# Kernel optimization log

Measured on AMD Instinct MI355X. Metric: run time of the kernel, lower is better.

## Reference

```python
import jax, jax.numpy as jnp
import numpy as np

H = 128   # hidden_size
B = 8
TQ = 512  # num queries
TK = 512  # num keys


def setup_inputs() -> dict:
    key = jax.random.key(0)
    ks = jax.random.split(key, 8)
    s = 1.0 / np.sqrt(H)  # torch Linear default init bound
    return {
        "queries": jax.random.normal(ks[0], (B, TQ, H), dtype=jnp.float32),
        "keys": jax.random.normal(ks[1], (B, TK, H), dtype=jnp.float32),
        "Wa_w": jax.random.uniform(ks[2], (H, H), jnp.float32, -s, s),
        "Wa_b": jax.random.uniform(ks[3], (H,), jnp.float32, -s, s),
        "Ua_w": jax.random.uniform(ks[4], (H, H), jnp.float32, -s, s),
        "Ua_b": jax.random.uniform(ks[5], (H,), jnp.float32, -s, s),
        "Va_w": jax.random.uniform(ks[6], (H,), jnp.float32, -s, s),
        "Va_b": jax.random.uniform(ks[7], (), jnp.float32, -s, s),
    }


def reference(queries, keys, Wa_w, Wa_b, Ua_w, Ua_b, Va_w, Va_b):
    # Linear projections (torch Linear: y = x @ W.T + b)
    q = queries @ Wa_w.T + Wa_b                  # (B, Tq, H)
    k = keys @ Ua_w.T + Ua_b                     # (B, Tk, H)
    # Additive (Bahdanau) scores with broadcast intermediate (B, Tq, Tk, H)
    e = jnp.tanh(q[:, :, None, :] + k[:, None, :, :])
    scores = jnp.einsum('bqkh,h->bqk', e, Va_w) + Va_b  # (B, Tq, Tk)
    weights = jax.nn.softmax(scores, axis=-1)            # softmax over keys
    contexts = jnp.einsum('bqk,bkh->bqh', weights, keys) # (B, Tq, H)
    return contexts, weights
```

## Files before the change

### kernel.cpp

```cpp
#include <hip/hip_runtime.h>
#include <hip/hip_bf16.h>
#include <stdint.h>

#define HD 128
#define NB 8
#define TQN 512
#define TKN 512
#define QT 8
#define KTILE 64
#define KSTR 132
#define QSTR 132
#define KBSTR 136

typedef __attribute__((ext_vector_type(8))) short short8;
typedef __attribute__((ext_vector_type(4))) float f32x4;

static __device__ __forceinline__ float lo16(uint32_t w){
  union { uint32_t i; float f; } v; v.i = w << 16; return v.f;
}
static __device__ __forceinline__ float hi16(uint32_t w){
  union { uint32_t i; float f; } v; v.i = w & 0xffff0000u; return v.f;
}
static __device__ __forceinline__ float bf2f(unsigned short u){
  union { uint32_t i; float f; } v; v.i = ((uint32_t)u) << 16; return v.f;
}
static __device__ __forceinline__ uint32_t f2bf(float f){
  union { float f; uint32_t i; } v; v.f = f;
  uint32_t u = v.i;
  u += 0x7fffu + ((u >> 16) & 1u);
  return u >> 16;
}
static __device__ __forceinline__ float tanh_acc(float x){
  float e = __builtin_amdgcn_exp2f(x * 2.8853900817779268f);
  return fmaf(-2.0f, __builtin_amdgcn_rcpf(e + 1.0f), 1.0f);
}
template<int CTRL>
static __device__ __forceinline__ float dpp_add(float x){
  union { float f; int i; } u; u.f = x;
  int y = __builtin_amdgcn_update_dpp(0, u.i, CTRL, 0xf, 0xf, true);
  union { int i; float f; } w; w.i = y;
  return x + w.f;
}
static __device__ __forceinline__ float ld1(const void* p, size_t idx, bool f32){
  return f32 ? ((const float*)p)[idx] : bf2f(((const unsigned short*)p)[idx]);
}
static __device__ __forceinline__ short8 ld8bf(const void* p, size_t idx, bool f32){
  short8 r;
  if (f32){
    const float* s = (const float*)p + idx;
    #pragma unroll
    for (int i = 0; i < 8; i++) r[i] = (short)f2bf(s[i]);
  } else {
    r = *(const short8*)((const unsigned short*)p + idx);
  }
  return r;
}

__global__ __launch_bounds__(256) void proj_kernel(
    const void* __restrict__ queries, const void* __restrict__ keys,
    const void* __restrict__ Wa_w,   const void* __restrict__ Wa_b,
    const void* __restrict__ Ua_w,   const void* __restrict__ Ua_b,
    float* __restrict__ tq_g, float* __restrict__ tk_g)
{
  __shared__ unsigned int flg_s[8];
  const int tid = threadIdx.x;
  if (tid < 8) flg_s[tid] = 0;
  __syncthreads();
  {
    const void* ptrs[6] = {queries, keys, Wa_w, Wa_b, Ua_w, Ua_b};
    const int grp = tid >> 5;
    const int l   = tid & 31;
    if (grp < 6){
      const unsigned short* p = (const unsigned short*)ptrs[grp];
      unsigned short a = p[2*l], c = p[64 + 2*l];
      if (((a >> 7) & 0xFF) > 0x90 || ((c >> 7) & 0xFF) > 0x90)
        atomicOr(&flg_s[grp], 1u);
    }
  }
  __syncthreads();
  const int lane = tid & 63, wv = tid >> 6, ln = lane & 15, quad = lane >> 4;
  const int row0 = blockIdx.x * 16;

  const void* x; const void* W; const void* bias; float* dst; int r;
  bool fx, fw, fb;
  if (row0 < NB*TQN){
    x = queries; W = Wa_w; bias = Wa_b; dst = tq_g; r = row0;
    fx = flg_s[0] != 0; fw = flg_s[2] != 0; fb = flg_s[3] != 0;
  } else {
    x = keys; W = Ua_w; bias = Ua_b; dst = tk_g; r = row0 - NB*TQN;
    fx = flg_s[1] != 0; fw = flg_s[4] != 0; fb = flg_s[5] != 0;
  }

  short8 a[4];
  #pragma unroll
  for (int ks = 0; ks < 4; ks++)
    a[ks] = ld8bf(x, (size_t)(r + ln)*HD + ks*32 + quad*8, fx);

  #pragma unroll
  for (int nt = 0; nt < 2; nt++){
    const int h0 = (2*wv + nt)*16;
    f32x4 c = {0.f,0.f,0.f,0.f};
    #pragma unroll
    for (int ks = 0; ks < 4; ks++)
      c = __builtin_amdgcn_mfma_f32_16x16x32_bf16(
            a[ks], ld8bf(W, (size_t)(h0 + ln)*HD + ks*32 + quad*8, fw), c, 0,0,0);
    const float wb = ld1(bias, h0 + ln, fb);
    #pragma unroll
    for (int r4 = 0; r4 < 4; r4++)
      dst[(size_t)(r + quad*4 + r4)*HD + h0 + ln] = tanh_acc(c[r4] + wb);
  }
}

__global__ __launch_bounds__(512, 6) void attn_kernel(
    const void* __restrict__ queries, const void* __restrict__ keys,
    const void* __restrict__ Va_w,
    const float* __restrict__ tq_g, const float* __restrict__ tk_g,
    void* __restrict__ out)
{
  __shared__ __align__(16) float tk_s[KTILE*KSTR];
  __shared__ float sc_s[QT*TKN];
  __shared__ unsigned int flg_s[4];

  const int tid = threadIdx.x;
  if (tid < 4) flg_s[tid] = 0;
  __syncthreads();
  {
    const void* ptrs[3] = {queries, keys, Va_w};
    const int grp = tid >> 5;
    const int l   = tid & 31;
    if (grp < 3){
      const unsigned short* p = (const unsigned short*)ptrs[grp];
      unsigned short a = p[2*l], c = p[64 + 2*l];
      if (((a >> 7) & 0xFF) > 0x90 || ((c >> 7) & 0xFF) > 0x90)
        atomicOr(&flg_s[grp], 1u);
    }
  }
  __syncthreads();
  const bool fQ  = flg_s[0] != 0;
  const bool fK  = flg_s[1] != 0;
  const bool fVw = flg_s[2] != 0;

  const int lane = tid & 63;
  const int wv   = tid >> 6;
  const int ln   = lane & 15;
  const int quad = lane >> 4;
  const int s8   = lane >> 3;
  const int o8   = lane & 7;
  const int b     = blockIdx.x >> 6;
  const int qbase = (blockIdx.x & 63) * QT;

  float var[16], tqr[16];
  {
    #pragma unroll
    for (int j = 0; j < 16; j++) var[j] = ld1(Va_w, o8*16 + j, fVw);
    const float4* qsrc = (const float4*)(tq_g + (size_t)(b*TQN + qbase + wv)*HD + o8*16);
    #pragma unroll
    for (int c = 0; c < 4; c++){
      float4 t = qsrc[c];
      tqr[c*4+0]=t.x; tqr[c*4+1]=t.y; tqr[c*4+2]=t.z; tqr[c*4+3]=t.w;
    }
  }

  float sc8[8];
  for (int kt = 0; kt < 8; kt++){
    {
      const float4* src = (const float4*)(tk_g + (size_t)(b*TKN + kt*KTILE)*HD);
      #pragma unroll
      for (int j = 0; j < 4; j++){
        const int f = tid + 512*j;
        const int k = f >> 5;
        const int h = (f & 31) * 4;
        *(float4*)(tk_s + k*KSTR + h) = src[f];
      }
    }
    __syncthreads();

    float acc[8];
    #pragma unroll
    for (int i = 0; i < 8; i++) acc[i] = 0.f;
    #pragma unroll
    for (int i = 0; i < 8; i++){
      const float* tk = tk_s + (i*8 + s8)*KSTR + o8*16;
      #pragma unroll
      for (int c = 0; c < 4; c++){
        const float4 kv = *(const float4*)(tk + c*4);
        acc[i] = fmaf(var[c*4+0]*(tqr[c*4+0]+kv.x),
                      __builtin_amdgcn_rcpf(fmaf(tqr[c*4+0], kv.x, 1.f)), acc[i]);
        acc[i] = fmaf(var[c*4+1]*(tqr[c*4+1]+kv.y),
                      __builtin_amdgcn_rcpf(fmaf(tqr[c*4+1], kv.y, 1.f)), acc[i]);
        acc[i] = fmaf(var[c*4+2]*(tqr[c*4+2]+kv.z),
                      __builtin_amdgcn_rcpf(fmaf(tqr[c*4+2], kv.z, 1.f)), acc[i]);
        acc[i] = fmaf(var[c*4+3]*(tqr[c*4+3]+kv.w),
                      __builtin_amdgcn_rcpf(fmaf(tqr[c*4+3], kv.w, 1.f)), acc[i]);
      }
    }
    #pragma unroll
    for (int i = 0; i < 8; i++){
      float a = acc[i];
      a = dpp_add<0xB1>(a);
      a = dpp_add<0x4E>(a);
      a = dpp_add<0x141>(a);
      acc[i] = a;
    }
    float sc = acc[0];
    #pragma unroll
    for (int i = 1; i < 8; i++) sc = (o8 == i) ? acc[i] : sc;
    sc8[kt] = sc;
    __syncthreads();
  }

  {
    float m = sc8[0];
    #pragma unroll
    for (int j = 1; j < 8; j++) m = fmaxf(m, sc8[j]);
    #pragma unroll
    for (int o = 32; o > 0; o >>= 1) m = fmaxf(m, __shfl_xor(m, o));
    float sum = 0.f;
    #pragma unroll
    for (int j = 0; j < 8; j++){
      sc8[j] = __builtin_amdgcn_exp2f((sc8[j]-m)*1.4426950408889634f);
      sum += sc8[j];
    }
    #pragma unroll
    for (int o = 32; o > 0; o >>= 1) sum += __shfl_xor(sum, o);
    const float inv = __builtin_amdgcn_rcpf(sum);
    const size_t wbase = (size_t)NB*TQN*HD + (size_t)(b*TQN + qbase + wv)*TKN;
    #pragma unroll
    for (int j = 0; j < 8; j++){
      const float w = sc8[j]*inv;
      const int kk = j*KTILE + o8*8 + s8;
      sc_s[wv*TKN + kk] = w;
      if (fQ) ((float*)out)[wbase + kk] = w;
      else    ((unsigned short*)out)[wbase + kk] = (unsigned short)f2bf(w);
    }
  }
  __syncthreads();

  {
    const int p2 = wv & 3;
    const int g2 = wv >> 2;
    const int h0 = ln * 8;
    float a0[8], a1[8];
    #pragma unroll
    for (int t = 0; t < 8; t++){ a0[t] = 0.f; a1[t] = 0.f; }
    for (int kt = 0; kt < 8; kt++){
      if (fK){
        const float4* src = (const float4*)((const float*)keys + (size_t)(b*TKN + kt*KTILE)*HD);
        #pragma unroll
        for (int j = 0; j < 4; j++){
          const int f = tid + 512*j;
          const int k = f >> 5;
          const int h = (f & 31) * 4;
          *(float4*)(tk_s + k*KSTR + h) = src[f];
        }
      } else {
        const uint4* src = (const uint4*)((const unsigned short*)keys + (size_t)(b*TKN + kt*KTILE)*HD);
        #pragma unroll
        for (int j = 0; j < 2; j++){
          const int f = tid + 512*j;
          const int k = f >> 4;
          const int h = (f & 15) * 8;
          uint4 v = src[f];
          float4 d0, d1;
          d0.x = lo16(v.x); d0.y = hi16(v.x); d0.z = lo16(v.y); d0.w = hi16(v.y);
          d1.x = lo16(v.z); d1.y = hi16(v.z); d1.z = lo16(v.w); d1.w = hi16(v.w);
          *(float4*)(tk_s + k*KSTR + h)     = d0;
          *(float4*)(tk_s + k*KSTR + h + 4) = d1;
        }
      }
      __syncthreads();
      const float* w0r = sc_s + (2*p2)*TKN + kt*KTILE + g2*32;
      const float* w1r = w0r + TKN;
      #pragma unroll
      for (int i = 0; i < 8; i++){
        const int k = i*4 + quad;
        const float w0 = w0r[k];
        const float w1 = w1r[k];
        const float* kr = tk_s + (g2*32 + k)*KSTR + h0;
        const float4 k0 = *(const float4*)(kr);
        const float4 k1 = *(const float4*)(kr + 4);
        a0[0]=fmaf(w0,k0.x,a0[0]); a0[1]=fmaf(w0,k0.y,a0[1]);
        a0[2]=fmaf(w0,k0.z,a0[2]); a0[3]=fmaf(w0,k0.w,a0[3]);
        a0[4]=fmaf(w0,k1.x,a0[4]); a0[5]=fmaf(w0,k1.y,a0[5]);
        a0[6]=fmaf(w0,k1.z,a0[6]); a0[7]=fmaf(w0,k1.w,a0[7]);
        a1[0]=fmaf(w1,k0.x,a1[0]); a1[1]=fmaf(w1,k0.y,a1[1]);
        a1[2]=fmaf(w1,k0.z,a1[2]); a1[3]=fmaf(w1,k0.w,a1[3]);
        a1[4]=fmaf(w1,k1.x,a1[4]); a1[5]=fmaf(w1,k1.y,a1[5]);
        a1[6]=fmaf(w1,k1.z,a1[6]); a1[7]=fmaf(w1,k1.w,a1[7]);
      }
      __syncthreads();
    }
    #pragma unroll
    for (int t = 0; t < 8; t++){
      a0[t] += __shfl_xor(a0[t], 16); a0[t] += __shfl_xor(a0[t], 32);
      a1[t] += __shfl_xor(a1[t], 16); a1[t] += __shfl_xor(a1[t], 32);
    }
    float* part = sc_s;
    if (g2 == 1 && quad == 0){
      *(float4*)(part + (2*p2  )*HD + h0    ) = (float4){a0[0],a0[1],a0[2],a0[3]};
      *(float4*)(part + (2*p2  )*HD + h0 + 4) = (float4){a0[4],a0[5],a0[6],a0[7]};
      *(float4*)(part + (2*p2+1)*HD + h0    ) = (float4){a1[0],a1[1],a1[2],a1[3]};
      *(float4*)(part + (2*p2+1)*HD + h0 + 4) = (float4){a1[4],a1[5],a1[6],a1[7]};
    }
    __syncthreads();
    if (g2 == 0 && quad == 0){
      const float4 p00 = *(const float4*)(part + (2*p2  )*HD + h0    );
      const float4 p01 = *(const float4*)(part + (2*p2  )*HD + h0 + 4);
      const float4 p10 = *(const float4*)(part + (2*p2+1)*HD + h0    );
      const float4 p11 = *(const float4*)(part + (2*p2+1)*HD + h0 + 4);
      const size_t crow0 = (size_t)(b*TQN + qbase + 2*p2    )*HD + h0;
      const size_t crow1 = (size_t)(b*TQN + qbase + 2*p2 + 1)*HD + h0;
      if (fQ){
        float* oc = (float*)out;
        *(float4*)(oc + crow0)     = (float4){a0[0]+p00.x, a0[1]+p00.y, a0[2]+p00.z, a0[3]+p00.w};
        *(float4*)(oc + crow0 + 4) = (float4){a0[4]+p01.x, a0[5]+p01.y, a0[6]+p01.z, a0[7]+p01.w};
        *(float4*)(oc + crow1)     = (float4){a1[0]+p10.x, a1[1]+p10.y, a1[2]+p10.z, a1[3]+p10.w};
        *(float4*)(oc + crow1 + 4) = (float4){a1[4]+p11.x, a1[5]+p11.y, a1[6]+p11.z, a1[7]+p11.w};
      } else {
        uint4 o0, o1;
        o0.x = f2bf(a0[0]+p00.x) | (f2bf(a0[1]+p00.y) << 16);
        o0.y = f2bf(a0[2]+p00.z) | (f2bf(a0[3]+p00.w) << 16);
        o0.z = f2bf(a0[4]+p01.x) | (f2bf(a0[5]+p01.y) << 16);
        o0.w = f2bf(a0[6]+p01.z) | (f2bf(a0[7]+p01.w) << 16);
        o1.x = f2bf(a1[0]+p10.x) | (f2bf(a1[1]+p10.y) << 16);
        o1.y = f2bf(a1[2]+p10.z) | (f2bf(a1[3]+p10.w) << 16);
        o1.z = f2bf(a1[4]+p11.x) | (f2bf(a1[5]+p11.y) << 16);
        o1.w = f2bf(a1[6]+p11.z) | (f2bf(a1[7]+p11.w) << 16);
        *(uint4*)((unsigned short*)out + crow0) = o0;
        *(uint4*)((unsigned short*)out + crow1) = o1;
      }
    }
  }
}

__global__ __launch_bounds__(512, 4) void fused_kernel(
    const void* __restrict__ queries, const void* __restrict__ keys,
    const void* __restrict__ Wa_w,   const void* __restrict__ Wa_b,
    const void* __restrict__ Ua_w,   const void* __restrict__ Ua_b,
    const void* __restrict__ Va_w,
    void* __restrict__ out)
{
  __shared__ float qp_s[QT*QSTR];
  __shared__ float va_s[HD];
  __shared__ __align__(16) unsigned short keys_s[KTILE*KBSTR];
  __shared__ __align__(16) float kp_s[KTILE*KSTR];
  __shared__ float sc_s[QT*TKN];
  __shared__ unsigned int flg_s[8];

  const int tid = threadIdx.x;
  if (tid < 8) flg_s[tid] = 0;
  __syncthreads();
  {
    const void* ptrs[7] = {queries, keys, Wa_w, Wa_b, Ua_w, Ua_b, Va_w};
    const int grp = tid >> 5;
    const int l   = tid & 31;
    if (grp < 7){
      const unsigned short* p = (const unsigned short*)ptrs[grp];
      unsigned short a = p[2*l], c = p[64 + 2*l];
      if (((a >> 7) & 0xFF) > 0x90 || ((c >> 7) & 0xFF) > 0x90)
        atomicOr(&flg_s[grp], 1u);
    }
  }
  __syncthreads();
  const bool fQ  = flg_s[0] != 0;
  const bool fK  = flg_s[1] != 0;
  const bool fWw = flg_s[2] != 0;
  const bool fWb = flg_s[3] != 0;
  const bool fUw = flg_s[4] != 0;
  const bool fUb = flg_s[5] != 0;
  const bool fVw = flg_s[6] != 0;

  const int lane = tid & 63;
  const int wv   = tid >> 6;
  const int ln   = lane & 15;
  const int quad = lane >> 4;
  const int b     = blockIdx.x >> 6;
  const int qbase = (blockIdx.x & 63) * QT;

  if (tid < HD) va_s[tid] = ld1(Va_w, tid, fVw);
  {
    const int h0 = wv * 16;
    const size_t qrow = (size_t)(b*TQN + qbase + (ln & 7))*HD;
    f32x4 c = {0.f,0.f,0.f,0.f};
    #pragma unroll
    for (int ks = 0; ks < 4; ks++){
      short8 a = ld8bf(queries, qrow + ks*32 + quad*8, fQ);
      short8 w = ld8bf(Wa_w, (size_t)(h0 + ln)*HD + ks*32 + quad*8, fWw);
      c = __builtin_amdgcn_mfma_f32_16x16x32_bf16(a, w, c, 0,0,0);
    }
    const float wb = ld1(Wa_b, h0 + ln, fWb);
    #pragma unroll
    for (int r = 0; r < 4; r++){
      const int row = quad*4 + r;
      if (row < QT) qp_s[row*QSTR + h0 + ln] = tanh_acc(c[r] + wb);
    }
  }
  short8 ub[4];
  float ubias;
  {
    const int h0 = wv * 16;
    #pragma unroll
    for (int ks = 0; ks < 4; ks++)
      ub[ks] = ld8bf(Ua_w, (size_t)(h0 + ln)*HD + ks*32 + quad*8, fUw);
    ubias = ld1(Ua_b, h0 + ln, fUb);
  }
  {
    if (fK){
      const float4* src = (const float4*)((const float*)keys + (size_t)(b*TKN)*HD);
      #pragma unroll
      for (int j = 0; j < 4; j++){
        const int f = tid + 512*j;
        float4 v = src[f];
        const int k = f >> 5, h = (f & 31)*4;
        uint2 p;
        p.x = f2bf(v.x) | (f2bf(v.y) << 16);
        p.y = f2bf(v.z) | (f2bf(v.w) << 16);
        *(uint2*)(keys_s + k*KBSTR + h) = p;
      }
    } else {
      const uint4* src = (const uint4*)((const unsigned short*)keys + (size_t)(b*TKN)*HD);
      #pragma unroll
      for (int j = 0; j < 2; j++){
        const int f = tid + 512*j;
        uint4 v = src[f];
        const int k = f >> 4, h = (f & 15)*8;
        *(uint4*)(keys_s + k*KBSTR + h) = v;
      }
    }
  }
  __syncthreads();

  const int s8 = lane >> 3;
  const int o8 = lane & 7;
  float tqr[16], var[16], vat[16];
  {
    const float* qsrc = qp_s + wv*QSTR + o8*16;
    const float* vsrc = va_s + o8*16;
    #pragma unroll
    for (int c = 0; c < 4; c++){
      float4 t = *(const float4*)(qsrc + c*4);
      float4 v = *(const float4*)(vsrc + c*4);
      tqr[c*4+0]=t.x; tqr[c*4+1]=t.y; tqr[c*4+2]=t.z; tqr[c*4+3]=t.w;
      var[c*4+0]=v.x; var[c*4+1]=v.y; var[c*4+2]=v.z; var[c*4+3]=v.w;
      vat[c*4+0]=v.x*t.x; vat[c*4+1]=v.y*t.y; vat[c*4+2]=v.z*t.z; vat[c*4+3]=v.w*t.w;
    }
  }
  for (int kt = 0; kt < 8; kt++){
    f32x4 kc[4];
    #pragma unroll
    for (int mt = 0; mt < 4; mt++) kc[mt] = (f32x4){0.f,0.f,0.f,0.f};
    #pragma unroll
    for (int ks = 0; ks < 4; ks++){
      short8 af[4];
      #pragma unroll
      for (int mt = 0; mt < 4; mt++)
        af[mt] = *(const short8*)(keys_s + (mt*16 + ln)*KBSTR + ks*32 + quad*8);
      #pragma unroll
      for (int mt = 0; mt < 4; mt++)
        kc[mt] = __builtin_amdgcn_mfma_f32_16x16x32_bf16(af[mt], ub[ks], kc[mt], 0,0,0);
    }
    __syncthreads();
    #pragma unroll
    for (int mt = 0; mt < 4; mt++)
      #pragma unroll
      for (int r = 0; r < 4; r++)
        kp_s[(mt*16 + quad*4 + r)*KSTR + wv*16 + ln] = tanh_acc(kc[mt][r] + ubias);
    if (kt < 7){
      if (fK){
        const float4* src = (const float4*)((const float*)keys + (size_t)(b*TKN + (kt+1)*KTILE)*HD);
        #pragma unroll
        for (int j = 0; j < 4; j++){
          const int f = tid + 512*j;
          float4 v = src[f];
          const int k = f >> 5, h = (f & 31)*4;
          uint2 p;
          p.x = f2bf(v.x) | (f2bf(v.y) << 16);
          p.y = f2bf(v.z) | (f2bf(v.w) << 16);
          *(uint2*)(keys_s + k*KBSTR + h) = p;
        }
      } else {
        const uint4* src = (const uint4*)((const unsigned short*)keys + (size_t)(b*TKN + (kt+1)*KTILE)*HD);
        #pragma unroll
        for (int j = 0; j < 2; j++){
          const int f = tid + 512*j;
          uint4 v = src[f];
          const int k = f >> 4, h = (f & 15)*8;
          *(uint4*)(keys_s + k*KBSTR + h) = v;
        }
      }
    }
    __syncthreads();
    float acc[8];
    #pragma unroll
    for (int i = 0; i < 8; i++) acc[i] = 0.f;
    #pragma unroll
    for (int i = 0; i < 8; i++){
      const float* tk = kp_s + (i*8 + s8)*KSTR + o8*16;
      #pragma unroll
      for (int c = 0; c < 4; c++){
        const float4 kv = *(const float4*)(tk + c*4);
        acc[i] = fmaf(fmaf(var[c*4+0], kv.x, vat[c*4+0]),
                      __builtin_amdgcn_rcpf(fmaf(tqr[c*4+0], kv.x, 1.f)), acc[i]);
        acc[i] = fmaf(fmaf(var[c*4+1], kv.y, vat[c*4+1]),
                      __builtin_amdgcn_rcpf(fmaf(tqr[c*4+1], kv.y, 1.f)), acc[i]);
        acc[i] = fmaf(fmaf(var[c*4+2], kv.z, vat[c*4+2]),
                      __builtin_amdgcn_rcpf(fmaf(tqr[c*4+2], kv.z, 1.f)), acc[i]);
        acc[i] = fmaf(fmaf(var[c*4+3], kv.w, vat[c*4+3]),
                      __builtin_amdgcn_rcpf(fmaf(tqr[c*4+3], kv.w, 1.f)), acc[i]);
      }
    }
    #pragma unroll
    for (int i = 0; i < 8; i++){
      float a = acc[i];
      a = dpp_add<0xB1>(a);
      a = dpp_add<0x4E>(a);
      a = dpp_add<0x141>(a);
      acc[i] = a;
    }
    float sc = acc[0];
    #pragma unroll
    for (int i = 1; i < 8; i++) sc = (o8 == i) ? acc[i] : sc;
    sc_s[wv*TKN + kt*KTILE + o8*8 + s8] = sc;
  }
  __syncthreads();
  {
    float vals[8];
    float m = -1e30f;
    #pragma unroll
    for (int j = 0; j < 8; j++){
      vals[j] = sc_s[wv*TKN + lane + 64*j];
      m = fmaxf(m, vals[j]);
    }
    #pragma unroll
    for (int o = 32; o > 0; o >>= 1) m = fmaxf(m, __shfl_xor(m, o));
    float sum = 0.f;
    #pragma unroll
    for (int j = 0; j < 8; j++){
      vals[j] = __builtin_amdgcn_exp2f((vals[j]-m)*1.4426950408889634f);
      sum += vals[j];
    }
    #pragma unroll
    for (int o = 32; o > 0; o >>= 1) sum += __shfl_xor(sum, o);
    const float inv = __builtin_amdgcn_rcpf(sum);
    const size_t wbase = (size_t)NB*TQN*HD + (size_t)(b*TQN + qbase + wv)*TKN;
    #pragma unroll
    for (int j = 0; j < 8; j++){
      const float w = vals[j]*inv;
      sc_s[wv*TKN + lane + 64*j] = w;
      if (fQ) ((float*)out)[wbase + lane + 64*j] = w;
      else    ((unsigned short*)out)[wbase + lane + 64*j] = (unsigned short)f2bf(w);
    }
  }
  __syncthreads();
  {
    const int p2 = wv & 3;
    const int g2 = wv >> 2;
    const int h0 = ln * 8;
    float a0[8], a1[8];
    #pragma unroll
    for (int t = 0; t < 8; t++){ a0[t] = 0.f; a1[t] = 0.f; }
    for (int kt = 0; kt < 8; kt++){
      if (fK){
        const float4* src = (const float4*)((const float*)keys + (size_t)(b*TKN + kt*KTILE)*HD);
        #pragma unroll
        for (int j = 0; j < 4; j++){
          const int f = tid + 512*j;
          const int k = f >> 5, h = (f & 31)*4;
          *(float4*)(kp_s + k*KSTR + h) = src[f];
        }
      } else {
        const uint4* src = (const uint4*)((const unsigned short*)keys + (size_t)(b*TKN + kt*KTILE)*HD);
        #pragma unroll
        for (int j = 0; j < 2; j++){
          const int f = tid + 512*j;
          const int k = f >> 4, h = (f & 15)*8;
          uint4 v = src[f];
          float4 d0, d1;
          d0.x = lo16(v.x); d0.y = hi16(v.x); d0.z = lo16(v.y); d0.w = hi16(v.y);
          d1.x = lo16(v.z); d1.y = hi16(v.z); d1.z = lo16(v.w); d1.w = hi16(v.w);
          *(float4*)(kp_s + k*KSTR + h)     = d0;
          *(float4*)(kp_s + k*KSTR + h + 4) = d1;
        }
      }
      __syncthreads();
      const float* w0r = sc_s + (2*p2)*TKN + kt*KTILE + g2*32;
      const float* w1r = w0r + TKN;
      #pragma unroll
      for (int i = 0; i < 8; i++){
        const int k = i*4 + quad;
        const float w0 = w0r[k];
        const float w1 = w1r[k];
        const float* kr = kp_s + (g2*32 + k)*KSTR + h0;
        const float4 k0 = *(const float4*)(kr);
        const float4 k1 = *(const float4*)(kr + 4);
        a0[0]=fmaf(w0,k0.x,a0[0]); a0[1]=fmaf(w0,k0.y,a0[1]);
        a0[2]=fmaf(w0,k0.z,a0[2]); a0[3]=fmaf(w0,k0.w,a0[3]);
        a0[4]=fmaf(w0,k1.x,a0[4]); a0[5]=fmaf(w0,k1.y,a0[5]);
        a0[6]=fmaf(w0,k1.z,a0[6]); a0[7]=fmaf(w0,k1.w,a0[7]);
        a1[0]=fmaf(w1,k0.x,a1[0]); a1[1]=fmaf(w1,k0.y,a1[1]);
        a1[2]=fmaf(w1,k0.z,a1[2]); a1[3]=fmaf(w1,k0.w,a1[3]);
        a1[4]=fmaf(w1,k1.x,a1[4]); a1[5]=fmaf(w1,k1.y,a1[5]);
        a1[6]=fmaf(w1,k1.z,a1[6]); a1[7]=fmaf(w1,k1.w,a1[7]);
      }
      __syncthreads();
    }
    #pragma unroll
    for (int t = 0; t < 8; t++){
      a0[t] += __shfl_xor(a0[t], 16); a0[t] += __shfl_xor(a0[t], 32);
      a1[t] += __shfl_xor(a1[t], 16); a1[t] += __shfl_xor(a1[t], 32);
    }
    float* part = qp_s;
    if (g2 == 1 && quad == 0){
      *(float4*)(part + (2*p2  )*HD + h0    ) = (float4){a0[0],a0[1],a0[2],a0[3]};
      *(float4*)(part + (2*p2  )*HD + h0 + 4) = (float4){a0[4],a0[5],a0[6],a0[7]};
      *(float4*)(part + (2*p2+1)*HD + h0    ) = (float4){a1[0],a1[1],a1[2],a1[3]};
      *(float4*)(part + (2*p2+1)*HD + h0 + 4) = (float4){a1[4],a1[5],a1[6],a1[7]};
    }
    __syncthreads();
    if (g2 == 0 && quad == 0){
      const float4 p00 = *(const float4*)(part + (2*p2  )*HD + h0    );
      const float4 p01 = *(const float4*)(part + (2*p2  )*HD + h0 + 4);
      const float4 p10 = *(const float4*)(part + (2*p2+1)*HD + h0    );
      const float4 p11 = *(const float4*)(part + (2*p2+1)*HD + h0 + 4);
      const size_t crow0 = (size_t)(b*TQN + qbase + 2*p2    )*HD + h0;
      const size_t crow1 = (size_t)(b*TQN + qbase + 2*p2 + 1)*HD + h0;
      if (fQ){
        float* oc = (float*)out;
        *(float4*)(oc + crow0)     = (float4){a0[0]+p00.x, a0[1]+p00.y, a0[2]+p00.z, a0[3]+p00.w};
        *(float4*)(oc + crow0 + 4) = (float4){a0[4]+p01.x, a0[5]+p01.y, a0[6]+p01.z, a0[7]+p01.w};
        *(float4*)(oc + crow1)     = (float4){a1[0]+p10.x, a1[1]+p10.y, a1[2]+p10.z, a1[3]+p10.w};
        *(float4*)(oc + crow1 + 4) = (float4){a1[4]+p11.x, a1[5]+p11.y, a1[6]+p11.z, a1[7]+p11.w};
      } else {
        uint4 o0, o1;
        o0.x = f2bf(a0[0]+p00.x) | (f2bf(a0[1]+p00.y) << 16);
        o0.y = f2bf(a0[2]+p00.z) | (f2bf(a0[3]+p00.w) << 16);
        o0.z = f2bf(a0[4]+p01.x) | (f2bf(a0[5]+p01.y) << 16);
        o0.w = f2bf(a0[6]+p01.z) | (f2bf(a0[7]+p01.w) << 16);
        o1.x = f2bf(a1[0]+p10.x) | (f2bf(a1[1]+p10.y) << 16);
        o1.y = f2bf(a1[2]+p10.z) | (f2bf(a1[3]+p10.w) << 16);
        o1.z = f2bf(a1[4]+p11.x) | (f2bf(a1[5]+p11.y) << 16);
        o1.w = f2bf(a1[6]+p11.z) | (f2bf(a1[7]+p11.w) << 16);
        *(uint4*)((unsigned short*)out + crow0) = o0;
        *(uint4*)((unsigned short*)out + crow1) = o1;
      }
    }
  }
}

extern "C" void kernel_launch(void* const* d_in, const int* in_sizes, int n_in,
                              void* d_out, int out_size, void* d_ws, size_t ws_size,
                              hipStream_t stream) {
  (void)in_sizes; (void)n_in; (void)out_size;
  const size_t need = (size_t)2 * NB * TQN * HD * sizeof(float);
  if (ws_size >= need){
    float* tq_g = (float*)d_ws;
    float* tk_g = tq_g + (size_t)NB*TQN*HD;
    proj_kernel<<<512, 256, 0, stream>>>(d_in[0], d_in[1], d_in[2], d_in[3],
                                         d_in[4], d_in[5], tq_g, tk_g);
    attn_kernel<<<512, 512, 0, stream>>>(d_in[0], d_in[1], d_in[6],
                                         tq_g, tk_g, d_out);
  } else {
    fused_kernel<<<512, 512, 0, stream>>>(d_in[0], d_in[1], d_in[2], d_in[3],
                                          d_in[4], d_in[5], d_in[6], d_out);
  }
}
```

Measured before the change: 156.0 us.

## Prefetch key tiles into registers, use packed FMA math, interleave batches across blocks

Tiles of projected keys and raw keys are now prefetched into registers while the current tile is being computed, so global loads overlap with compute. The score and context inner loops use two-wide float vectors, which lets the compiler emit packed FMA, and the score numerator is algebraically refactored to var*k + var*q. Block indexing is interleaved by batch, softmax weights are transposed with ds_bpermute to give coalesced stores, and the occupancy hint drops from 6 to 4 blocks to leave registers for the prefetch buffers. The risks are higher register pressure and lower occupancy.

```diff
diff --git a/kernel.cpp b/kernel.cpp
--- a/kernel.cpp
+++ b/kernel.cpp
@@ -14,6 +14,13 @@
 
 typedef __attribute__((ext_vector_type(8))) short short8;
 typedef __attribute__((ext_vector_type(4))) float f32x4;
+typedef __attribute__((ext_vector_type(2))) float f32x2;
+
+#if __has_builtin(__builtin_elementwise_fma)
+#define FMA2(a,b,c) __builtin_elementwise_fma((a),(b),(c))
+#else
+#define FMA2(a,b,c) ((a)*(b)+(c))
+#endif
 
 static __device__ __forceinline__ float lo16(uint32_t w){
   union { uint32_t i; float f; } v; v.i = w << 16; return v.f;
@@ -79,7 +86,10 @@
   }
   __syncthreads();
   const int lane = tid & 63, wv = tid >> 6, ln = lane & 15, quad = lane >> 4;
-  const int row0 = blockIdx.x * 16;
+  const int b7  = blockIdx.x & 7;
+  const int idx = blockIdx.x >> 3;
+  const int row0 = (idx < 32) ? (b7*TQN + idx*16)
+                              : (NB*TQN + b7*TKN + (idx-32)*16);
 
   const void* x; const void* W; const void* bias; float* dst; int r;
   bool fx, fw, fb;
@@ -111,7 +121,7 @@
   }
 }
 
-__global__ __launch_bounds__(512, 6) void attn_kernel(
+__global__ __launch_bounds__(512, 4) void attn_kernel(
     const void* __restrict__ queries, const void* __restrict__ keys,
     const void* __restrict__ Va_w,
     const float* __restrict__ tq_g, const float* __restrict__ tk_g,
@@ -122,6 +132,16 @@
   __shared__ unsigned int flg_s[4];
 
   const int tid = threadIdx.x;
+  const int b     = blockIdx.x & 7;
+  const int qbase = (blockIdx.x >> 3) * QT;
+
+  float4 st[4];
+  {
+    const float4* src = (const float4*)(tk_g + (size_t)(b*TKN)*HD);
+    #pragma unroll
+    for (int j = 0; j < 4; j++) st[j] = src[tid + 512*j];
+  }
+
   if (tid < 4) flg_s[tid] = 0;
   __syncthreads();
   {
@@ -146,67 +166,87 @@
   const int quad = lane >> 4;
   const int s8   = lane >> 3;
   const int o8   = lane & 7;
-  const int b     = blockIdx.x >> 6;
-  const int qbase = (blockIdx.x & 63) * QT;
-
-  float var[16], tqr[16];
-  {
-    #pragma unroll
-    for (int j = 0; j < 16; j++) var[j] = ld1(Va_w, o8*16 + j, fVw);
+
+  f32x2 var2[8], tq2[8], vat2[8];
+  {
+    float vtmp[16];
+    #pragma unroll
+    for (int j = 0; j < 16; j++) vtmp[j] = ld1(Va_w, o8*16 + j, fVw);
     const float4* qsrc = (const float4*)(tq_g + (size_t)(b*TQN + qbase + wv)*HD + o8*16);
     #pragma unroll
     for (int c = 0; c < 4; c++){
       float4 t = qsrc[c];
-      tqr[c*4+0]=t.x; tqr[c*4+1]=t.y; tqr[c*4+2]=t.z; tqr[c*4+3]=t.w;
-    }
-  }
+      f32x2 t0; t0.x = t.x; t0.y = t.y;
+      f32x2 t1; t1.x = t.z; t1.y = t.w;
+      f32x2 v0; v0.x = vtmp[4*c+0]; v0.y = vtmp[4*c+1];
+      f32x2 v1; v1.x = vtmp[4*c+2]; v1.y = vtmp[4*c+3];
+      tq2[2*c] = t0;  tq2[2*c+1] = t1;
+      var2[2*c] = v0; var2[2*c+1] = v1;
+      vat2[2*c] = v0 * t0; vat2[2*c+1] = v1 * t1;
+    }
+  }
+  f32x2 one2; one2.x = 1.f; one2.y = 1.f;
 
   float sc8[8];
   for (int kt = 0; kt < 8; kt++){
-    {
-      const float4* src = (const float4*)(tk_g + (size_t)(b*TKN + kt*KTILE)*HD);
-      #pragma unroll
-      for (int j = 0; j < 4; j++){
-        const int f = tid + 512*j;
-        const int k = f >> 5;
-        const int h = (f & 31) * 4;
-        *(float4*)(tk_s + k*KSTR + h) = src[f];
-      }
+    #pragma unroll
+    for (int j = 0; j < 4; j++){
+      const int f = tid + 512*j;
+      *(float4*)(tk_s + (f >> 5)*KSTR + (f & 31)*4) = st[j];
     }
     __syncthreads();
-
-    float acc[8];
-    #pragma unroll
-    for (int i = 0; i < 8; i++) acc[i] = 0.f;
+    if (kt < 7){
+      const float4* src = (const float4*)(tk_g + (size_t)(b*TKN + (kt+1)*KTILE)*HD);
+      #pragma unroll
+      for (int j = 0; j < 4; j++) st[j] = src[tid + 512*j];
+    }
+
+    f32x2 acc2[8];
+    #pragma unroll
+    for (int i = 0; i < 8; i++){ acc2[i].x = 0.f; acc2[i].y = 0.f; }
     #pragma unroll
     for (int i = 0; i < 8; i++){
       const float* tk = tk_s + (i*8 + s8)*KSTR + o8*16;
       #pragma unroll
       for (int c = 0; c < 4; c++){
         const float4 kv = *(const float4*)(tk + c*4);
-        acc[i] = fmaf(var[c*4+0]*(tqr[c*4+0]+kv.x),
-                      __builtin_amdgcn_rcpf(fmaf(tqr[c*4+0], kv.x, 1.f)), acc[i]);
-        acc[i] = fmaf(var[c*4+1]*(tqr[c*4+1]+kv.y),
-                      __builtin_amdgcn_rcpf(fmaf(tqr[c*4+1], kv.y, 1.f)), acc[i]);
-        acc[i] = fmaf(var[c*4+2]*(tqr[c*4+2]+kv.z),
-                      __builtin_amdgcn_rcpf(fmaf(tqr[c*4+2], kv.z, 1.f)), acc[i]);
-        acc[i] = fmaf(var[c*4+3]*(tqr[c*4+3]+kv.w),
-                      __builtin_amdgcn_rcpf(fmaf(tqr[c*4+3], kv.w, 1.f)), acc[i]);
-      }
-    }
+        f32x2 kv0; kv0.x = kv.x; kv0.y = kv.y;
+        f32x2 kv1; kv1.x = kv.z; kv1.y = kv.w;
+        f32x2 n0 = FMA2(var2[2*c],   kv0, vat2[2*c]);
+        f32x2 d0 = FMA2(tq2[2*c],    kv0, one2);
+        f32x2 n1 = FMA2(var2[2*c+1], kv1, vat2[2*c+1]);
+        f32x2 d1 = FMA2(tq2[2*c+1],  kv1, one2);
+        f32x2 r0; r0.x = __builtin_amdgcn_rcpf(d0.x); r0.y = __builtin_amdgcn_rcpf(d0.y);
+        f32x2 r1; r1.x = __builtin_amdgcn_rcpf(d1.x); r1.y = __builtin_amdgcn_rcpf(d1.y);
+        acc2[i] = FMA2(n0, r0, acc2[i]);
+        acc2[i] = FMA2(n1, r1, acc2[i]);
+      }
+    }
+    float ar[8];
     #pragma unroll
     for (int i = 0; i < 8; i++){
-      float a = acc[i];
+      float a = acc2[i].x + acc2[i].y;
       a = dpp_add<0xB1>(a);
       a = dpp_add<0x4E>(a);
       a = dpp_add<0x141>(a);
-      acc[i] = a;
-    }
-    float sc = acc[0];
-    #pragma unroll
-    for (int i = 1; i < 8; i++) sc = (o8 == i) ? acc[i] : sc;
+      ar[i] = a;
+    }
+    float sc = ar[0];
+    #pragma unroll
+    for (int i = 1; i < 8; i++) sc = (o8 == i) ? ar[i] : sc;
     sc8[kt] = sc;
     __syncthreads();
+  }
+
+  uint4 kf[4];
+  if (fK){
+    const uint4* src = (const uint4*)((const float*)keys + (size_t)(b*TKN)*HD);
+    #pragma unroll
+    for (int j = 0; j < 4; j++) kf[j] = src[tid + 512*j];
+  } else {
+    const uint4* src = (const uint4*)((const unsigned short*)keys + (size_t)(b*TKN)*HD);
+    #pragma unroll
+    for (int j = 0; j < 2; j++) kf[j] = src[tid + 512*j];
   }
 
   {
@@ -224,14 +264,15 @@
     #pragma unroll
     for (int o = 32; o > 0; o >>= 1) sum += __shfl_xor(sum, o);
     const float inv = __builtin_amdgcn_rcpf(sum);
+    const int psrc = ((((lane & 7) << 3) | (lane >> 3)) << 2);
     const size_t wbase = (size_t)NB*TQN*HD + (size_t)(b*TQN + qbase + wv)*TKN;
     #pragma unroll
     for (int j = 0; j < 8; j++){
-      const float w = sc8[j]*inv;
-      const int kk = j*KTILE + o8*8 + s8;
-      sc_s[wv*TKN + kk] = w;
-      if (fQ) ((float*)out)[wbase + kk] = w;
-      else    ((unsigned short*)out)[wbase + kk] = (unsigned short)f2bf(w);
+      union { float f; int i; } u; u.f = sc8[j]*inv;
+      union { int i; float f; } t; t.i = __builtin_amdgcn_ds_bpermute(psrc, u.i);
+      sc_s[wv*TKN + j*64 + lane] = t.f;
+      if (fQ) ((float*)out)[wbase + j*64 + lane] = t.f;
+      else    ((unsigned short*)out)[wbase + j*64 + lane] = (unsigned short)f2bf(t.f);
     }
   }
   __syncthreads();
@@ -240,27 +281,29 @@
     const int p2 = wv & 3;
     const int g2 = wv >> 2;
     const int h0 = ln * 8;
-    float a0[8], a1[8];
-    #pragma unroll
-    for (int t = 0; t < 8; t++){ a0[t] = 0.f; a1[t] = 0.f; }
+    f32x2 a0v[4], a1v[4];
+    #pragma unroll
+    for (int t = 0; t < 4; t++){
+      a0v[t].x = 0.f; a0v[t].y = 0.f;
+      a1v[t].x = 0.f; a1v[t].y = 0.f;
+    }
     for (int kt = 0; kt < 8; kt++){
       if (fK){
-        const float4* src = (const float4*)((const float*)keys + (size_t)(b*TKN + kt*KTILE)*HD);
         #pragma unroll
         for (int j = 0; j < 4; j++){
           const int f = tid + 512*j;
-          const int k = f >> 5;
-          const int h = (f & 31) * 4;
-          *(float4*)(tk_s + k*KSTR + h) = src[f];
+          float4 v;
+          v.x = __uint_as_float(kf[j].x); v.y = __uint_as_float(kf[j].y);
+          v.z = __uint_as_float(kf[j].z); v.w = __uint_as_float(kf[j].w);
+          *(float4*)(tk_s + (f >> 5)*KSTR + (f & 31)*4) = v;
         }
       } else {
-        const uint4* src = (const uint4*)((const unsigned short*)keys + (size_t)(b*TKN + kt*KTILE)*HD);
         #pragma unroll
         for (int j = 0; j < 2; j++){
           const int f = tid + 512*j;
           const int k = f >> 4;
           const int h = (f & 15) * 8;
-          uint4 v = src[f];
+          uint4 v = kf[j];
           float4 d0, d1;
           d0.x = lo16(v.x); d0.y = hi16(v.x); d0.z = lo16(v.y); d0.w = hi16(v.y);
           d1.x = lo16(v.z); d1.y = hi16(v.z); d1.z = lo16(v.w); d1.w = hi16(v.w);
@@ -269,6 +312,17 @@
         }
       }
       __syncthreads();
+      if (kt < 7){
+        if (fK){
+          const uint4* src = (const uint4*)((const float*)keys + (size_t)(b*TKN + (kt+1)*KTILE)*HD);
+          #pragma unroll
+          for (int j = 0; j < 4; j++) kf[j] = src[tid + 512*j];
+        } else {
+          const uint4* src = (const uint4*)((const unsigned short*)keys + (size_t)(b*TKN + (kt+1)*KTILE)*HD);
+          #pragma unroll
+          for (int j = 0; j < 2; j++) kf[j] = src[tid + 512*j];
+        }
+      }
       const float* w0r = sc_s + (2*p2)*TKN + kt*KTILE + g2*32;
       const float* w1r = w0r + TKN;
       #pragma unroll
@@ -279,16 +333,24 @@
         const float* kr = tk_s + (g2*32 + k)*KSTR + h0;
         const float4 k0 = *(const float4*)(kr);
         const float4 k1 = *(const float4*)(kr + 4);
-        a0[0]=fmaf(w0,k0.x,a0[0]); a0[1]=fmaf(w0,k0.y,a0[1]);
-        a0[2]=fmaf(w0,k0.z,a0[2]); a0[3]=fmaf(w0,k0.w,a0[3]);
-        a0[4]=fmaf(w0,k1.x,a0[4]); a0[5]=fmaf(w0,k1.y,a0[5]);
-        a0[6]=fmaf(w0,k1.z,a0[6]); a0[7]=fmaf(w0,k1.w,a0[7]);
-        a1[0]=fmaf(w1,k0.x,a1[0]); a1[1]=fmaf(w1,k0.y,a1[1]);
-        a1[2]=fmaf(w1,k0.z,a1[2]); a1[3]=fmaf(w1,k0.w,a1[3]);
-        a1[4]=fmaf(w1,k1.x,a1[4]); a1[5]=fmaf(w1,k1.y,a1[5]);
-        a1[6]=fmaf(w1,k1.z,a1[6]); a1[7]=fmaf(w1,k1.w,a1[7]);
+        f32x2 c0; c0.x = k0.x; c0.y = k0.y;
+        f32x2 c1; c1.x = k0.z; c1.y = k0.w;
+        f32x2 c2; c2.x = k1.x; c2.y = k1.y;
+        f32x2 c3; c3.x = k1.z; c3.y = k1.w;
+        f32x2 w0v; w0v.x = w0; w0v.y = w0;
+        f32x2 w1v; w1v.x = w1; w1v.y = w1;
+        a0v[0] = FMA2(w0v, c0, a0v[0]); a0v[1] = FMA2(w0v, c1, a0v[1]);
+        a0v[2] = FMA2(w0v, c2, a0v[2]); a0v[3] = FMA2(w0v, c3, a0v[3]);
+        a1v[0] = FMA2(w1v, c0, a1v[0]); a1v[1] = FMA2(w1v, c1, a1v[1]);
+        a1v[2] = FMA2(w1v, c2, a1v[2]); a1v[3] = FMA2(w1v, c3, a1v[3]);
       }
       __syncthreads();
+    }
+    float a0[8], a1[8];
+    #pragma unroll
+    for (int t = 0; t < 4; t++){
+      a0[2*t] = a0v[t].x; a0[2*t+1] = a0v[t].y;
+      a1[2*t] = a1v[t].x; a1[2*t+1] = a1v[t].y;
     }
     #pragma unroll
     for (int t = 0; t < 8; t++){
```

After: 149.2 us. 4.4% less time.
